# Optimization experiments

Hardware: AMD Instinct MI355X
Metric: run time of the kernel (lower is better)

The kernel has to match this reference:

```python
import jax, jax.numpy as jnp
import numpy as np

N_NODES = 100000
N_EDGES = 1600000
N_GRAPHS = 1000
D_IN = 64
D_HID = 64
D_OUT = 8


def _glorot(k, shape):
    lim = float(np.sqrt(6.0 / (shape[0] + shape[1])))
    return jax.random.uniform(k, shape, jnp.float32, -lim, lim)


def setup_inputs() -> dict:
    key = jax.random.key(0)
    ks = jax.random.split(key, 12)
    x = jax.random.normal(ks[0], (N_NODES, D_IN), jnp.float32)
    edge_index = jax.random.randint(ks[1], (2, N_EDGES), 0, N_NODES, jnp.int32)
    batch = jnp.sort(jax.random.randint(ks[2], (N_NODES,), 0, N_GRAPHS, jnp.int32))
    return {
        "x": x,
        "edge_index": edge_index,
        "batch": batch,
        "W1": _glorot(ks[3], (D_IN, D_HID)),
        "b1": jnp.zeros((D_HID,), jnp.float32),
        "W2": _glorot(ks[4], (D_HID, D_HID)),
        "b2": jnp.zeros((D_HID,), jnp.float32),
        "lw1": _glorot(ks[5], (D_HID, D_HID // 2)),
        "lb1": jnp.zeros((D_HID // 2,), jnp.float32),
        "lw2": _glorot(ks[6], (D_HID // 2, D_OUT)),
        "lb2": jnp.zeros((D_OUT,), jnp.float32),
    }


def reference(x, edge_index, batch, W1, b1, W2, b2, lw1, lb1, lw2, lb2):
    # --- GCN normalization (PyG defaults: add self-loops, sym norm) ---
    loop = jnp.arange(N_NODES, dtype=edge_index.dtype)
    src = jnp.concatenate([edge_index[0], loop])
    dst = jnp.concatenate([edge_index[1], loop])
    deg = jax.ops.segment_sum(jnp.ones_like(dst, jnp.float32), dst, num_segments=N_NODES)
    dinv = jnp.where(deg > 0, jax.lax.rsqrt(jnp.maximum(deg, 1.0)), 0.0)
    norm = dinv[src] * dinv[dst]  # [E+N]

    def gcn_conv(h, W, b):
        h = h @ W  # [N, d]
        msg = h[src] * norm[:, None]  # gather along edges
        return jax.ops.segment_sum(msg, dst, num_segments=N_NODES) + b

    h = jax.nn.relu(gcn_conv(x, W1, b1))
    h = gcn_conv(h, W2, b2)

    # --- global mean pool per graph ---
    counts = jax.ops.segment_sum(jnp.ones((N_NODES,), jnp.float32), batch, num_segments=N_GRAPHS)
    pooled = jax.ops.segment_sum(h, batch, num_segments=N_GRAPHS) / jnp.maximum(counts, 1.0)[:, None]

    # --- MLP head (dropout = identity in eval) ---
    z = jax.nn.relu(pooled @ lw1 + lb1)
    return z @ lw2 + lb2
```

## Files before the change

### kernel.cpp

```cpp
#include <hip/hip_runtime.h>

static constexpr int NN  = 100000;
static constexpr int NE  = 1600000;
static constexpr int NG  = 1000;
static constexpr int D   = 64;
static constexpr int DH  = 32;
static constexpr int DO  = 8;
static constexpr int BKT = 128;
static constexpr int NBK = (NN + BKT - 1) / BKT;
static constexpr int CAP = 2560;
static constexpr int CHUNK = 4096;
static constexpr int NCH = (NE + CHUNK - 1) / CHUNK;

typedef __attribute__((ext_vector_type(8))) short bf16x8;
typedef __attribute__((ext_vector_type(4))) float f32x4;

__device__ __forceinline__ float b2f(unsigned short u) {
    return __uint_as_float(((unsigned int)u) << 16);
}
__device__ __forceinline__ unsigned short f2b(float f) {
    unsigned int u = __float_as_uint(f);
    u += 0x7FFFu + ((u >> 16) & 1u);
    return (unsigned short)(u >> 16);
}
__device__ __forceinline__ uint4 pack8(const unsigned short* h) {
    uint4 u;
    u.x = (unsigned)h[0] | ((unsigned)h[1] << 16);
    u.y = (unsigned)h[2] | ((unsigned)h[3] << 16);
    u.z = (unsigned)h[4] | ((unsigned)h[5] << 16);
    u.w = (unsigned)h[6] | ((unsigned)h[7] << 16);
    return u;
}

__global__ __launch_bounds__(256) void
k_prepw(const float* __restrict__ W1, const float* __restrict__ W2,
        unsigned short* __restrict__ wtbuf, int* __restrict__ gcur) {
    int t = threadIdx.x;
    if (blockIdx.x == 0) {
        for (int b = t; b < NBK; b += 256) gcur[b] = 0;
    } else {
        const float* W = (blockIdx.x == 2) ? W2 : W1;
        unsigned short* WtHi = wtbuf + (size_t)(blockIdx.x - 1) * 8192;
        unsigned short* WtLo = WtHi + 4096;
        int n = t >> 2, k0 = (t & 3) * 16;
        unsigned short hi[16], lo[16];
#pragma unroll
        for (int i = 0; i < 16; ++i) {
            float v = W[(k0 + i) * 64 + n];
            hi[i] = f2b(v);
            lo[i] = f2b(v - b2f(hi[i]));
        }
        ((uint4*)WtHi)[n * 8 + (t & 3) * 2]     = pack8(hi);
        ((uint4*)WtHi)[n * 8 + (t & 3) * 2 + 1] = pack8(hi + 8);
        ((uint4*)WtLo)[n * 8 + (t & 3) * 2]     = pack8(lo);
        ((uint4*)WtLo)[n * 8 + (t & 3) * 2 + 1] = pack8(lo + 8);
    }
}

__global__ __launch_bounds__(512) void
k_bin(const int* __restrict__ src, const int* __restrict__ dst,
      int* __restrict__ gcur, int* __restrict__ ebuf) {
    __shared__ int lcnt[NBK];
    __shared__ int lbase[NBK];
    int t = threadIdx.x;
    long base = (long)blockIdx.x * CHUNK;
    for (int b = t; b < NBK; b += 512) lcnt[b] = 0;
    __syncthreads();
    int pk[8], bk[8], of[8];
#pragma unroll
    for (int j = 0; j < 8; ++j) {
        long i = base + j * 512 + t;
        if (i < NE) {
            int d = dst[i];
            bk[j] = d >> 7;
            pk[j] = src[i] * BKT + (d & (BKT - 1));
            of[j] = atomicAdd(&lcnt[bk[j]], 1);
        } else bk[j] = -1;
    }
    __syncthreads();
    for (int b = t; b < NBK; b += 512) {
        int c = lcnt[b];
        if (c) lbase[b] = b * CAP + atomicAdd(&gcur[b], c);
    }
    __syncthreads();
#pragma unroll
    for (int j = 0; j < 8; ++j)
        if (bk[j] >= 0) ebuf[lbase[bk[j]] + of[j]] = pk[j];
}

__global__ __launch_bounds__(512) void
k_csrdeg(const int* __restrict__ gcur, const int* __restrict__ ebuf,
         int* __restrict__ rowptr, int* __restrict__ deg, float* __restrict__ dinv,
         int* __restrict__ csr) {
    __shared__ int hist[BKT];
    __shared__ int sc[BKT];
    __shared__ int lcur[BKT];
    int b = blockIdx.x, t = threadIdx.x;
    if (t < BKT) hist[t] = 0;
    __syncthreads();
    int beg = b * CAP;
    int end = beg + gcur[b];
    for (int e = beg + t; e < end; e += 512)
        atomicAdd(&hist[ebuf[e] & (BKT - 1)], 1);
    __syncthreads();
    if (t < BKT) sc[t] = hist[t];
    __syncthreads();
    for (int o = 1; o < BKT; o <<= 1) {
        int a = (t < BKT && t >= o) ? sc[t - o] : 0;
        __syncthreads();
        if (t < BKT) sc[t] += a;
        __syncthreads();
    }
    int v0 = b * BKT;
    if (t < BKT) {
        int v = v0 + t;
        if (v < NN) {
            int excl = beg + sc[t] - hist[t];
            rowptr[v] = excl;
            deg[v]    = hist[t];
            dinv[v]   = rsqrtf((float)(hist[t] + 1));
            lcur[t]   = excl;
        }
    }
    __syncthreads();
    for (int e = beg + t; e < end; e += 512) {
        int p = ebuf[e];
        int slot = atomicAdd(&lcur[p & (BKT - 1)], 1);
        csr[slot] = p >> 7;
    }
}

__global__ __launch_bounds__(256) void
k_mm_mfma(const float* __restrict__ Ain, const unsigned short* __restrict__ wt,
          const float* __restrict__ dinv, uint4* __restrict__ out) {
    __shared__ unsigned short smem[4 * 64 * 72];
    unsigned short* Ahi  = smem;
    unsigned short* Alo  = smem + 4608;
    unsigned short* WtHi = smem + 9216;
    unsigned short* WtLo = smem + 13824;
    int t = threadIdx.x;
    int r = t >> 2, cc = t & 3, c0 = cc * 16;
    long n0 = (long)blockIdx.x * 64;
    {
        const uint4* H = (const uint4*)wt;
        const uint4* L = (const uint4*)(wt + 4096);
        uint4* dh = (uint4*)&WtHi[r * 72 + c0];
        uint4* dl = (uint4*)&WtLo[r * 72 + c0];
        dh[0] = H[r * 8 + cc * 2]; dh[1] = H[r * 8 + cc * 2 + 1];
        dl[0] = L[r * 8 + cc * 2]; dl[1] = L[r * 8 + cc * 2 + 1];
    }
    {
        long n = n0 + r; if (n >= NN) n = NN - 1;
        const float4* X = (const float4*)Ain;
        unsigned short hi[16], lo[16];
#pragma unroll
        for (int i = 0; i < 4; ++i) {
            float4 v = X[n * 16 + cc * 4 + i];
            float vv[4] = {v.x, v.y, v.z, v.w};
#pragma unroll
            for (int j = 0; j < 4; ++j) {
                unsigned short h = f2b(vv[j]);
                hi[i * 4 + j] = h;
                lo[i * 4 + j] = f2b(vv[j] - b2f(h));
            }
        }
        uint4* dh = (uint4*)&Ahi[r * 72 + c0];
        uint4* dl = (uint4*)&Alo[r * 72 + c0];
        dh[0] = pack8(hi); dh[1] = pack8(hi + 8);
        dl[0] = pack8(lo); dl[1] = pack8(lo + 8);
    }
    __syncthreads();
    int lane = t & 63, w = t >> 6;
    int q = lane >> 4, m = lane & 15;
    f32x4 acc[4] = {{0.f,0.f,0.f,0.f},{0.f,0.f,0.f,0.f},{0.f,0.f,0.f,0.f},{0.f,0.f,0.f,0.f}};
#pragma unroll
    for (int s = 0; s < 2; ++s) {
        int ko = s * 32 + q * 8;
        bf16x8 ah = *(const bf16x8*)&Ahi[(w * 16 + m) * 72 + ko];
        bf16x8 al = *(const bf16x8*)&Alo[(w * 16 + m) * 72 + ko];
#pragma unroll
        for (int c = 0; c < 4; ++c) {
            bf16x8 bh = *(const bf16x8*)&WtHi[(c * 16 + m) * 72 + ko];
            bf16x8 bl = *(const bf16x8*)&WtLo[(c * 16 + m) * 72 + ko];
            acc[c] = __builtin_amdgcn_mfma_f32_16x16x32_bf16(ah, bh, acc[c], 0, 0, 0);
            acc[c] = __builtin_amdgcn_mfma_f32_16x16x32_bf16(ah, bl, acc[c], 0, 0, 0);
            acc[c] = __builtin_amdgcn_mfma_f32_16x16x32_bf16(al, bh, acc[c], 0, 0, 0);
        }
    }
    __syncthreads();
    float* Ct = (float*)smem;
#pragma unroll
    for (int c = 0; c < 4; ++c)
#pragma unroll
        for (int rr = 0; rr < 4; ++rr)
            Ct[(w * 16 + q * 4 + rr) * 68 + c * 16 + m] = acc[c][rr];
    __syncthreads();
    {
        long n = n0 + r;
        if (n < NN) {
            float dv = dinv[n];
            unsigned short ob[16];
#pragma unroll
            for (int i = 0; i < 4; ++i) {
                float4 v = *(const float4*)&Ct[r * 68 + c0 + i * 4];
                ob[i * 4 + 0] = f2b(v.x * dv); ob[i * 4 + 1] = f2b(v.y * dv);
                ob[i * 4 + 2] = f2b(v.z * dv); ob[i * 4 + 3] = f2b(v.w * dv);
            }
            out[n * 8 + cc * 2]     = pack8(ob);
            out[n * 8 + cc * 2 + 1] = pack8(ob + 8);
        }
    }
}

__global__ __launch_bounds__(512) void
k_aggmm(const int* __restrict__ rowptr, const int* __restrict__ deg,
        const int* __restrict__ csr,
        const uint4* __restrict__ g4, const float* __restrict__ dinv,
        const float* __restrict__ bias, const unsigned short* __restrict__ wt,
        uint4* __restrict__ out) {
    __shared__ unsigned short smem[3 * 4608];
    unsigned short* Ahi  = smem;
    unsigned short* WtHi = smem + 4608;
    unsigned short* WtLo = smem + 9216;
    int t = threadIdx.x;
    long n0 = (long)blockIdx.x * 64;
    if (t < 256) {
        int r = t >> 2, cc = t & 3, c0 = cc * 16;
        const uint4* H = (const uint4*)wt;
        const uint4* L = (const uint4*)(wt + 4096);
        uint4* dh = (uint4*)&WtHi[r * 72 + c0];
        uint4* dl = (uint4*)&WtLo[r * 72 + c0];
        dh[0] = H[r * 8 + cc * 2]; dh[1] = H[r * 8 + cc * 2 + 1];
        dl[0] = L[r * 8 + cc * 2]; dl[1] = L[r * 8 + cc * 2 + 1];
    }
    int lane = t & 63, w = t >> 6;
    int fg = lane & 7, slot = lane >> 3;
    int ln = w * 8 + slot;
    long v = n0 + ln;
    int vc = (v < NN) ? (int)v : NN - 1;
    int beg = rowptr[vc];
    int len = (v < NN) ? deg[vc] : 0;
    int lmax = len;
    lmax = max(lmax, __shfl_xor(lmax, 8));
    lmax = max(lmax, __shfl_xor(lmax, 16));
    lmax = max(lmax, __shfl_xor(lmax, 32));
    float acc[8];
    {
        uint4 sv = g4[(long)vc * 8 + fg];
        if (v >= NN) { sv.x = sv.y = sv.z = sv.w = 0u; }
        acc[0] = __uint_as_float(sv.x << 16); acc[1] = __uint_as_float(sv.x & 0xFFFF0000u);
        acc[2] = __uint_as_float(sv.y << 16); acc[3] = __uint_as_float(sv.y & 0xFFFF0000u);
        acc[4] = __uint_as_float(sv.z << 16); acc[5] = __uint_as_float(sv.z & 0xFFFF0000u);
        acc[6] = __uint_as_float(sv.w << 16); acc[7] = __uint_as_float(sv.w & 0xFFFF0000u);
    }
    for (int e = 0; e < lmax; e += 8) {
#pragma unroll
        for (int j = 0; j < 8; ++j) {
            int ee = e + j;
            float m = (ee < len) ? 1.f : 0.f;
            int idx = beg + ((ee < len) ? ee : 0);
            int srcn = csr[idx];
            uint4 a = g4[(long)srcn * 8 + fg];
            acc[0] += m * __uint_as_float(a.x << 16);
            acc[1] += m * __uint_as_float(a.x & 0xFFFF0000u);
            acc[2] += m * __uint_as_float(a.y << 16);
            acc[3] += m * __uint_as_float(a.y & 0xFFFF0000u);
            acc[4] += m * __uint_as_float(a.z << 16);
            acc[5] += m * __uint_as_float(a.z & 0xFFFF0000u);
            acc[6] += m * __uint_as_float(a.w << 16);
            acc[7] += m * __uint_as_float(a.w & 0xFFFF0000u);
        }
    }
    {
        float dv = dinv[vc];
        unsigned short ob[8];
#pragma unroll
        for (int k = 0; k < 8; ++k) {
            float x = fmaxf(acc[k] * dv + bias[fg * 8 + k], 0.f);
            ob[k] = f2b(x);
        }
        *(uint4*)&Ahi[ln * 72 + fg * 8] = pack8(ob);
    }
    __syncthreads();
    int q = lane >> 4, m = lane & 15;
    int rs = (w & 3) * 16;
    int cb0 = (w >> 2) * 2;
    f32x4 c2[2] = {{0.f,0.f,0.f,0.f},{0.f,0.f,0.f,0.f}};
#pragma unroll
    for (int s = 0; s < 2; ++s) {
        int ko = s * 32 + q * 8;
        bf16x8 ah = *(const bf16x8*)&Ahi[(rs + m) * 72 + ko];
#pragma unroll
        for (int c = 0; c < 2; ++c) {
            bf16x8 bh = *(const bf16x8*)&WtHi[((cb0 + c) * 16 + m) * 72 + ko];
            bf16x8 bl = *(const bf16x8*)&WtLo[((cb0 + c) * 16 + m) * 72 + ko];
            c2[c] = __builtin_amdgcn_mfma_f32_16x16x32_bf16(ah, bh, c2[c], 0, 0, 0);
            c2[c] = __builtin_amdgcn_mfma_f32_16x16x32_bf16(ah, bl, c2[c], 0, 0, 0);
        }
    }
    __syncthreads();
    float* Ct = (float*)smem;
#pragma unroll
    for (int c = 0; c < 2; ++c)
#pragma unroll
        for (int rr = 0; rr < 4; ++rr)
            Ct[(rs + q * 4 + rr) * 68 + (cb0 + c) * 16 + m] = c2[c][rr];
    __syncthreads();
    {
        int r = t >> 3, c8 = (t & 7) * 8;
        long n = n0 + r;
        if (n < NN) {
            float dv = dinv[n];
            float4 a = *(const float4*)&Ct[r * 68 + c8];
            float4 b = *(const float4*)&Ct[r * 68 + c8 + 4];
            unsigned short ob[8] = {f2b(a.x * dv), f2b(a.y * dv), f2b(a.z * dv), f2b(a.w * dv),
                                    f2b(b.x * dv), f2b(b.y * dv), f2b(b.z * dv), f2b(b.w * dv)};
            out[n * 8 + (t & 7)] = pack8(ob);
        }
    }
}

__global__ __launch_bounds__(256) void
k_agg2(const int* __restrict__ rowptr, const int* __restrict__ deg,
       const int* __restrict__ csr,
       const uint4* __restrict__ g4, const float* __restrict__ dinv,
       const float* __restrict__ bias, uint4* __restrict__ out4) {
    int t = threadIdx.x;
    int lane = t & 63;
    int fg = lane & 7;
    int slot = lane >> 3;
    int wid = blockIdx.x * 4 + (t >> 6);
    int v = wid * 8 + slot;
    int beg = rowptr[v];
    int len = deg[v];
    int lmax = len;
    lmax = max(lmax, __shfl_xor(lmax, 8));
    lmax = max(lmax, __shfl_xor(lmax, 16));
    lmax = max(lmax, __shfl_xor(lmax, 32));
    float acc[8];
    {
        uint4 sv = g4[(long)v * 8 + fg];
        acc[0] = __uint_as_float(sv.x << 16); acc[1] = __uint_as_float(sv.x & 0xFFFF0000u);
        acc[2] = __uint_as_float(sv.y << 16); acc[3] = __uint_as_float(sv.y & 0xFFFF0000u);
        acc[4] = __uint_as_float(sv.z << 16); acc[5] = __uint_as_float(sv.z & 0xFFFF0000u);
        acc[6] = __uint_as_float(sv.w << 16); acc[7] = __uint_as_float(sv.w & 0xFFFF0000u);
    }
    for (int e = 0; e < lmax; e += 8) {
#pragma unroll
        for (int j = 0; j < 8; ++j) {
            int ee = e + j;
            float m = (ee < len) ? 1.f : 0.f;
            int idx = beg + ((ee < len) ? ee : 0);
            int srcn = csr[idx];
            uint4 a = g4[(long)srcn * 8 + fg];
            acc[0] += m * __uint_as_float(a.x << 16);
            acc[1] += m * __uint_as_float(a.x & 0xFFFF0000u);
            acc[2] += m * __uint_as_float(a.y << 16);
            acc[3] += m * __uint_as_float(a.y & 0xFFFF0000u);
            acc[4] += m * __uint_as_float(a.z << 16);
            acc[5] += m * __uint_as_float(a.z & 0xFFFF0000u);
            acc[6] += m * __uint_as_float(a.w << 16);
            acc[7] += m * __uint_as_float(a.w & 0xFFFF0000u);
        }
    }
    float dv = dinv[v];
    unsigned short ob[8];
#pragma unroll
    for (int k = 0; k < 8; ++k)
        ob[k] = f2b(acc[k] * dv + bias[fg * 8 + k]);
    out4[(long)v * 8 + fg] = pack8(ob);
}

__global__ void k_poolhead(const unsigned short* __restrict__ h,
                           const int* __restrict__ batch,
                           const float* __restrict__ lw1, const float* __restrict__ lb1,
                           const float* __restrict__ lw2, const float* __restrict__ lb2,
                           float* __restrict__ out) {
    __shared__ float pl[D];
    __shared__ float z[DH];
    int g = blockIdx.x;
    int t = threadIdx.x;
    int lo = 0, hi = NN;
    while (lo < hi) { int m = (lo + hi) >> 1; if (batch[m] < g) lo = m + 1; else hi = m; }
    int lb = lo;
    hi = NN;
    while (lo < hi) { int m = (lo + hi) >> 1; if (batch[m] < g + 1) lo = m + 1; else hi = m; }
    int ub = lo;
    float s = 0.f;
    int n = lb;
    for (; n + 4 <= ub; n += 4) {
        float a0 = b2f(h[(long)(n + 0) * D + t]);
        float a1 = b2f(h[(long)(n + 1) * D + t]);
        float a2 = b2f(h[(long)(n + 2) * D + t]);
        float a3 = b2f(h[(long)(n + 3) * D + t]);
        s += a0 + a1 + a2 + a3;
    }
    for (; n < ub; ++n) s += b2f(h[(long)n * D + t]);
    pl[t] = s / fmaxf((float)(ub - lb), 1.0f);
    __syncthreads();
    if (t < DH) {
        float a = lb1[t];
#pragma unroll
        for (int k = 0; k < D; ++k) a += pl[k] * lw1[k * DH + t];
        z[t] = fmaxf(a, 0.f);
    }
    __syncthreads();
    if (t < DO) {
        float a = lb2[t];
#pragma unroll
        for (int j = 0; j < DH; ++j) a += z[j] * lw2[j * DO + t];
        out[g * DO + t] = a;
    }
}

extern "C" void kernel_launch(void* const* d_in, const int* in_sizes, int n_in,
                              void* d_out, int out_size, void* d_ws, size_t ws_size,
                              hipStream_t stream) {
    const float* x    = (const float*)d_in[0];
    const int*   ei   = (const int*)  d_in[1];
    const int*   batch= (const int*)  d_in[2];
    const float* W1   = (const float*)d_in[3];
    const float* b1   = (const float*)d_in[4];
    const float* W2   = (const float*)d_in[5];
    const float* b2   = (const float*)d_in[6];
    const float* lw1  = (const float*)d_in[7];
    const float* lb1  = (const float*)d_in[8];
    const float* lw2  = (const float*)d_in[9];
    const float* lb2  = (const float*)d_in[10];
    float* out = (float*)d_out;

    const int* srcv = ei;
    const int* dstv = ei + NE;

    char* ws = (char*)d_ws;
    size_t off = 0;
    auto alloc = [&](size_t bytes) {
        void* p = ws + off;
        off = (off + bytes + 255) & ~(size_t)255;
        return p;
    };
    int*   gcur   = (int*)  alloc((size_t)NBK * 4);
    int*   rowptr = (int*)  alloc((size_t)NN * 4);
    int*   deg    = (int*)  alloc((size_t)NN * 4);
    int*   csr    = (int*)  alloc((size_t)NBK * CAP * 4);
    float* dinv   = (float*)alloc((size_t)NN * 4);
    unsigned short* wtbuf = (unsigned short*)alloc((size_t)4 * 4096 * 2);
    unsigned short* bufA = (unsigned short*)alloc((size_t)NN * D * 2);
    unsigned short* bufB = (unsigned short*)alloc((size_t)NN * D * 2);
    int*   ebuf   = (int*)bufA;

    k_prepw <<<3, 256, 0, stream>>>(W1, W2, wtbuf, gcur);
    k_bin   <<<NCH, 512, 0, stream>>>(srcv, dstv, gcur, ebuf);
    k_csrdeg<<<NBK, 512, 0, stream>>>(gcur, ebuf, rowptr, deg, dinv, csr);

    const int MMB = (NN + 63) / 64;

    k_mm_mfma<<<MMB, 256, 0, stream>>>(x, wtbuf, dinv, (uint4*)bufA);
    k_aggmm<<<MMB, 512, 0, stream>>>(rowptr, deg, csr, (const uint4*)bufA, dinv, b1,
                                     wtbuf + 8192, (uint4*)bufB);
    k_agg2<<<NN / 32, 256, 0, stream>>>(rowptr, deg, csr, (const uint4*)bufB, dinv, b2,
                                        (uint4*)bufA);
    k_poolhead<<<NG, 64, 0, stream>>>(bufA, batch, lw1, lb1, lw2, lb2, out);
}
```

Measured before the change: 213.6 us.

## Sort nodes by degree within graphs and fuse second aggregation with mean pooling

Adds a per-graph counting sort of nodes by in-degree so that each wavefront in the aggregation kernels processes nodes of similar degree, reducing divergence from the padded lmax loop. The second aggregation now scales by dinv and accumulates directly into a pooled fp32 buffer with wave-level reduction and atomics, which removes the bf16 h2 write and the separate pool pass; b2 is folded into the head. This costs an extra sort kernel, indirect perm lookups, scattered output writes, and float atomics whose summation order is nondeterministic.

```diff
diff --git a/kernel.cpp b/kernel.cpp
--- a/kernel.cpp
+++ b/kernel.cpp
@@ -34,10 +34,16 @@
 
 __global__ __launch_bounds__(256) void
 k_prepw(const float* __restrict__ W1, const float* __restrict__ W2,
-        unsigned short* __restrict__ wtbuf, int* __restrict__ gcur) {
+        unsigned short* __restrict__ wtbuf, int* __restrict__ gcur,
+        float* __restrict__ pooled) {
     int t = threadIdx.x;
     if (blockIdx.x == 0) {
         for (int b = t; b < NBK; b += 256) gcur[b] = 0;
+    } else if (blockIdx.x >= 3) {
+        int b = blockIdx.x - 3;
+        float4 z4 = {0.f, 0.f, 0.f, 0.f};
+        for (int i = b * 256 + t; i < NG * D / 4; i += 8 * 256)
+            ((float4*)pooled)[i] = z4;
     } else {
         const float* W = (blockIdx.x == 2) ? W2 : W1;
         unsigned short* WtHi = wtbuf + (size_t)(blockIdx.x - 1) * 8192;
@@ -127,6 +133,45 @@
         int p = ebuf[e];
         int slot = atomicAdd(&lcur[p & (BKT - 1)], 1);
         csr[slot] = p >> 7;
+    }
+}
+
+__global__ __launch_bounds__(256) void
+k_gsort(const int* __restrict__ batch, const int* __restrict__ deg,
+        int* __restrict__ perm, int* __restrict__ cnts) {
+    __shared__ int hist[64];
+    __shared__ int scan[64];
+    __shared__ int bnd[2];
+    int g = blockIdx.x, t = threadIdx.x;
+    if (t < 2) {
+        int tgt = g + t;
+        int lo = 0, hi = NN;
+        while (lo < hi) { int m = (lo + hi) >> 1; if (batch[m] < tgt) lo = m + 1; else hi = m; }
+        bnd[t] = lo;
+    }
+    if (t < 64) hist[t] = 0;
+    __syncthreads();
+    int lb = bnd[0], ub = bnd[1], cnt = ub - lb;
+    if (t == 0) cnts[g] = cnt;
+    for (int i = t; i < cnt; i += 256) {
+        int d = deg[lb + i]; if (d > 63) d = 63;
+        atomicAdd(&hist[d], 1);
+    }
+    __syncthreads();
+    if (t < 64) scan[t] = hist[t];
+    __syncthreads();
+    for (int o = 1; o < 64; o <<= 1) {
+        int a = (t < 64 && t >= o) ? scan[t - o] : 0;
+        __syncthreads();
+        if (t < 64) scan[t] += a;
+        __syncthreads();
+    }
+    if (t < 64) hist[t] = scan[t] - hist[t];
+    __syncthreads();
+    for (int i = t; i < cnt; i += 256) {
+        int d = deg[lb + i]; if (d > 63) d = 63;
+        int pos = atomicAdd(&hist[d], 1);
+        perm[lb + pos] = lb + i;
     }
 }
 
@@ -217,7 +262,7 @@
         const int* __restrict__ csr,
         const uint4* __restrict__ g4, const float* __restrict__ dinv,
         const float* __restrict__ bias, const unsigned short* __restrict__ wt,
-        uint4* __restrict__ out) {
+        const int* __restrict__ perm, uint4* __restrict__ out) {
     __shared__ unsigned short smem[3 * 4608];
     unsigned short* Ahi  = smem;
     unsigned short* WtHi = smem + 4608;
@@ -237,7 +282,7 @@
     int fg = lane & 7, slot = lane >> 3;
     int ln = w * 8 + slot;
     long v = n0 + ln;
-    int vc = (v < NN) ? (int)v : NN - 1;
+    int vc = (v < NN) ? perm[v] : 0;
     int beg = rowptr[vc];
     int len = (v < NN) ? deg[vc] : 0;
     int lmax = len;
@@ -310,27 +355,29 @@
         int r = t >> 3, c8 = (t & 7) * 8;
         long n = n0 + r;
         if (n < NN) {
-            float dv = dinv[n];
+            int node = perm[n];
+            float dv = dinv[node];
             float4 a = *(const float4*)&Ct[r * 68 + c8];
             float4 b = *(const float4*)&Ct[r * 68 + c8 + 4];
             unsigned short ob[8] = {f2b(a.x * dv), f2b(a.y * dv), f2b(a.z * dv), f2b(a.w * dv),
                                     f2b(b.x * dv), f2b(b.y * dv), f2b(b.z * dv), f2b(b.w * dv)};
-            out[n * 8 + (t & 7)] = pack8(ob);
+            out[(long)node * 8 + (t & 7)] = pack8(ob);
         }
     }
 }
 
 __global__ __launch_bounds__(256) void
-k_agg2(const int* __restrict__ rowptr, const int* __restrict__ deg,
-       const int* __restrict__ csr,
-       const uint4* __restrict__ g4, const float* __restrict__ dinv,
-       const float* __restrict__ bias, uint4* __restrict__ out4) {
+k_agg2pool(const int* __restrict__ rowptr, const int* __restrict__ deg,
+           const int* __restrict__ csr,
+           const uint4* __restrict__ g4, const float* __restrict__ dinv,
+           const int* __restrict__ perm, const int* __restrict__ batch,
+           float* __restrict__ pooled) {
     int t = threadIdx.x;
     int lane = t & 63;
     int fg = lane & 7;
     int slot = lane >> 3;
-    int wid = blockIdx.x * 4 + (t >> 6);
-    int v = wid * 8 + slot;
+    int idx = blockIdx.x * 32 + (t >> 6) * 8 + slot;
+    int v = perm[idx];
     int beg = rowptr[v];
     int len = deg[v];
     int lmax = len;
@@ -350,8 +397,8 @@
         for (int j = 0; j < 8; ++j) {
             int ee = e + j;
             float m = (ee < len) ? 1.f : 0.f;
-            int idx = beg + ((ee < len) ? ee : 0);
-            int srcn = csr[idx];
+            int idx2 = beg + ((ee < len) ? ee : 0);
+            int srcn = csr[idx2];
             uint4 a = g4[(long)srcn * 8 + fg];
             acc[0] += m * __uint_as_float(a.x << 16);
             acc[1] += m * __uint_as_float(a.x & 0xFFFF0000u);
@@ -364,39 +411,40 @@
         }
     }
     float dv = dinv[v];
-    unsigned short ob[8];
-#pragma unroll
-    for (int k = 0; k < 8; ++k)
-        ob[k] = f2b(acc[k] * dv + bias[fg * 8 + k]);
-    out4[(long)v * 8 + fg] = pack8(ob);
-}
-
-__global__ void k_poolhead(const unsigned short* __restrict__ h,
-                           const int* __restrict__ batch,
-                           const float* __restrict__ lw1, const float* __restrict__ lb1,
-                           const float* __restrict__ lw2, const float* __restrict__ lb2,
-                           float* __restrict__ out) {
+#pragma unroll
+    for (int k = 0; k < 8; ++k) acc[k] *= dv;
+    int g = batch[v];
+    int g0 = __shfl(g, 0), g7 = __shfl(g, 63);
+    if (g0 == g7) {
+#pragma unroll
+        for (int k = 0; k < 8; ++k) {
+            acc[k] += __shfl_xor(acc[k], 8);
+            acc[k] += __shfl_xor(acc[k], 16);
+            acc[k] += __shfl_xor(acc[k], 32);
+        }
+        if (slot == 0) {
+#pragma unroll
+            for (int k = 0; k < 8; ++k)
+                atomicAdd(&pooled[g0 * D + fg * 8 + k], acc[k]);
+        }
+    } else {
+#pragma unroll
+        for (int k = 0; k < 8; ++k)
+            atomicAdd(&pooled[g * D + fg * 8 + k], acc[k]);
+    }
+}
+
+__global__ void k_head(const float* __restrict__ pooled, const int* __restrict__ cnts,
+                       const float* __restrict__ b2,
+                       const float* __restrict__ lw1, const float* __restrict__ lb1,
+                       const float* __restrict__ lw2, const float* __restrict__ lb2,
+                       float* __restrict__ out) {
     __shared__ float pl[D];
     __shared__ float z[DH];
     int g = blockIdx.x;
     int t = threadIdx.x;
-    int lo = 0, hi = NN;
-    while (lo < hi) { int m = (lo + hi) >> 1; if (batch[m] < g) lo = m + 1; else hi = m; }
-    int lb = lo;
-    hi = NN;
-    while (lo < hi) { int m = (lo + hi) >> 1; if (batch[m] < g + 1) lo = m + 1; else hi = m; }
-    int ub = lo;
-    float s = 0.f;
-    int n = lb;
-    for (; n + 4 <= ub; n += 4) {
-        float a0 = b2f(h[(long)(n + 0) * D + t]);
-        float a1 = b2f(h[(long)(n + 1) * D + t]);
-        float a2 = b2f(h[(long)(n + 2) * D + t]);
-        float a3 = b2f(h[(long)(n + 3) * D + t]);
-        s += a0 + a1 + a2 + a3;
-    }
-    for (; n < ub; ++n) s += b2f(h[(long)n * D + t]);
-    pl[t] = s / fmaxf((float)(ub - lb), 1.0f);
+    int c = cnts[g];
+    pl[t] = (c > 0) ? (pooled[g * D + t] / (float)c + b2[t]) : 0.f;
     __syncthreads();
     if (t < DH) {
         float a = lb1[t];
@@ -444,21 +492,25 @@
     int*   deg    = (int*)  alloc((size_t)NN * 4);
     int*   csr    = (int*)  alloc((size_t)NBK * CAP * 4);
     float* dinv   = (float*)alloc((size_t)NN * 4);
+    int*   perm   = (int*)  alloc((size_t)NN * 4);
+    int*   cnts   = (int*)  alloc((size_t)NG * 4);
+    float* pooled = (float*)alloc((size_t)NG * D * 4);
     unsigned short* wtbuf = (unsigned short*)alloc((size_t)4 * 4096 * 2);
     unsigned short* bufA = (unsigned short*)alloc((size_t)NN * D * 2);
     unsigned short* bufB = (unsigned short*)alloc((size_t)NN * D * 2);
     int*   ebuf   = (int*)bufA;
 
-    k_prepw <<<3, 256, 0, stream>>>(W1, W2, wtbuf, gcur);
+    k_prepw <<<11, 256, 0, stream>>>(W1, W2, wtbuf, gcur, pooled);
     k_bin   <<<NCH, 512, 0, stream>>>(srcv, dstv, gcur, ebuf);
     k_csrdeg<<<NBK, 512, 0, stream>>>(gcur, ebuf, rowptr, deg, dinv, csr);
+    k_gsort <<<NG, 256, 0, stream>>>(batch, deg, perm, cnts);
 
     const int MMB = (NN + 63) / 64;
 
     k_mm_mfma<<<MMB, 256, 0, stream>>>(x, wtbuf, dinv, (uint4*)bufA);
     k_aggmm<<<MMB, 512, 0, stream>>>(rowptr, deg, csr, (const uint4*)bufA, dinv, b1,
-                                     wtbuf + 8192, (uint4*)bufB);
-    k_agg2<<<NN / 32, 256, 0, stream>>>(rowptr, deg, csr, (const uint4*)bufB, dinv, b2,
-                                        (uint4*)bufA);
-    k_poolhead<<<NG, 64, 0, stream>>>(bufA, batch, lw1, lb1, lw2, lb2, out);
-}
+                                     wtbuf + 8192, perm, (uint4*)bufB);
+    k_agg2pool<<<NN / 32, 256, 0, stream>>>(rowptr, deg, csr, (const uint4*)bufB, dinv,
+                                            perm, batch, pooled);
+    k_head<<<NG, 64, 0, stream>>>(pooled, cnts, b2, lw1, lb1, lw2, lb2, out);
+}
```

After: 244.8 us. 1.15x slower.

## Fuse second GCN aggregation with per-graph mean pooling via graph-aligned wave map

Applied to the files above, without the earlier changes.

Builds a map assigning nodes to waves so each 8-node wave group belongs to a single graph (padded with -1), computed from batch boundaries in the prep kernel plus a new fill kernel. The second aggregation then reduces its 8 node results per wave with shuffles and writes a per-wave partial sum, and the head kernel sums partials per graph and adds the bias. This removes the bf16 write and reread of the full second-layer output and the per-graph binary searches in the pooling kernel. In exchange it adds an extra launch, padding waves, and a fixed MAXW capacity that assumes the padded wave count fits.

```diff
diff --git a/kernel.cpp b/kernel.cpp
--- a/kernel.cpp
+++ b/kernel.cpp
@@ -11,6 +11,8 @@
 static constexpr int CAP = 2560;
 static constexpr int CHUNK = 4096;
 static constexpr int NCH = (NE + CHUNK - 1) / CHUNK;
+static constexpr int MAXW = 13504;
+static constexpr int MAPS = MAXW * 8;
 
 typedef __attribute__((ext_vector_type(8))) short bf16x8;
 typedef __attribute__((ext_vector_type(4))) float f32x4;
@@ -32,29 +34,85 @@
     return u;
 }
 
-__global__ __launch_bounds__(256) void
+__global__ __launch_bounds__(1024) void
 k_prepw(const float* __restrict__ W1, const float* __restrict__ W2,
-        unsigned short* __restrict__ wtbuf, int* __restrict__ gcur) {
+        const int* __restrict__ batch,
+        unsigned short* __restrict__ wtbuf, int* __restrict__ gcur,
+        int* __restrict__ lbg, int* __restrict__ wbase, int* __restrict__ map) {
+    __shared__ int bnd[NG + 1];
+    __shared__ int tsum[256];
     int t = threadIdx.x;
-    if (blockIdx.x == 0) {
-        for (int b = t; b < NBK; b += 256) gcur[b] = 0;
+    int b = blockIdx.x;
+    if (b == 0) {
+        for (int i = t; i < NBK; i += 1024) gcur[i] = 0;
+    } else if (b == 3) {
+        for (int g = t; g <= NG; g += 1024) {
+            int lo = 0, hi = NN;
+            while (lo < hi) { int m = (lo + hi) >> 1; if (batch[m] < g) lo = m + 1; else hi = m; }
+            bnd[g] = lo;
+        }
+        __syncthreads();
+        int s = 0, loc[4];
+        if (t < 256) {
+#pragma unroll
+            for (int j = 0; j < 4; ++j) {
+                int g = t * 4 + j;
+                int pw = (g < NG) ? ((bnd[g + 1] - bnd[g] + 7) >> 3) : 0;
+                loc[j] = s; s += pw;
+            }
+            tsum[t] = s;
+        }
+        __syncthreads();
+        for (int o = 1; o < 256; o <<= 1) {
+            int a = (t < 256 && t >= o) ? tsum[t - o] : 0;
+            __syncthreads();
+            if (t < 256) tsum[t] += a;
+            __syncthreads();
+        }
+        if (t < 256) {
+            int base = (t > 0) ? tsum[t - 1] : 0;
+#pragma unroll
+            for (int j = 0; j < 4; ++j) {
+                int g = t * 4 + j;
+                if (g < NG) wbase[g] = base + loc[j];
+            }
+            if (t == 255) wbase[NG] = tsum[255];
+        }
+        if (t <= NG) lbg[t] = bnd[t];
+    } else if (b >= 4) {
+        int4 m4 = {-1, -1, -1, -1};
+        for (int i = (b - 4) * 1024 + t; i < MAPS / 4; i += 8 * 1024)
+            ((int4*)map)[i] = m4;
     } else {
-        const float* W = (blockIdx.x == 2) ? W2 : W1;
-        unsigned short* WtHi = wtbuf + (size_t)(blockIdx.x - 1) * 8192;
-        unsigned short* WtLo = WtHi + 4096;
-        int n = t >> 2, k0 = (t & 3) * 16;
-        unsigned short hi[16], lo[16];
-#pragma unroll
-        for (int i = 0; i < 16; ++i) {
-            float v = W[(k0 + i) * 64 + n];
-            hi[i] = f2b(v);
-            lo[i] = f2b(v - b2f(hi[i]));
-        }
-        ((uint4*)WtHi)[n * 8 + (t & 3) * 2]     = pack8(hi);
-        ((uint4*)WtHi)[n * 8 + (t & 3) * 2 + 1] = pack8(hi + 8);
-        ((uint4*)WtLo)[n * 8 + (t & 3) * 2]     = pack8(lo);
-        ((uint4*)WtLo)[n * 8 + (t & 3) * 2 + 1] = pack8(lo + 8);
-    }
+        if (t < 256) {
+            const float* W = (b == 2) ? W2 : W1;
+            unsigned short* WtHi = wtbuf + (size_t)(b - 1) * 8192;
+            unsigned short* WtLo = WtHi + 4096;
+            int n = t >> 2, k0 = (t & 3) * 16;
+            unsigned short hi[16], lo[16];
+#pragma unroll
+            for (int i = 0; i < 16; ++i) {
+                float v = W[(k0 + i) * 64 + n];
+                hi[i] = f2b(v);
+                lo[i] = f2b(v - b2f(hi[i]));
+            }
+            ((uint4*)WtHi)[n * 8 + (t & 3) * 2]     = pack8(hi);
+            ((uint4*)WtHi)[n * 8 + (t & 3) * 2 + 1] = pack8(hi + 8);
+            ((uint4*)WtLo)[n * 8 + (t & 3) * 2]     = pack8(lo);
+            ((uint4*)WtLo)[n * 8 + (t & 3) * 2 + 1] = pack8(lo + 8);
+        }
+    }
+}
+
+__global__ __launch_bounds__(128) void
+k_fillmap(const int* __restrict__ lbg, const int* __restrict__ wbase,
+          int* __restrict__ map) {
+    int g = blockIdx.x;
+    int base = wbase[g] * 8;
+    int lb = lbg[g], n = lbg[g + 1] - lb;
+    int padded = (n + 7) & ~7;
+    for (int i = threadIdx.x; i < padded; i += 128)
+        map[base + i] = (i < n) ? (lb + i) : -1;
 }
 
 __global__ __launch_bounds__(512) void
@@ -321,25 +379,27 @@
 }
 
 __global__ __launch_bounds__(256) void
-k_agg2(const int* __restrict__ rowptr, const int* __restrict__ deg,
-       const int* __restrict__ csr,
-       const uint4* __restrict__ g4, const float* __restrict__ dinv,
-       const float* __restrict__ bias, uint4* __restrict__ out4) {
+k_agg2pool(const int* __restrict__ rowptr, const int* __restrict__ deg,
+           const int* __restrict__ csr,
+           const uint4* __restrict__ g4, const float* __restrict__ dinv,
+           const int* __restrict__ map, float* __restrict__ partial) {
     int t = threadIdx.x;
     int lane = t & 63;
     int fg = lane & 7;
     int slot = lane >> 3;
-    int wid = blockIdx.x * 4 + (t >> 6);
-    int v = wid * 8 + slot;
-    int beg = rowptr[v];
-    int len = deg[v];
+    int w = blockIdx.x * 4 + (t >> 6);
+    int v = map[w * 8 + slot];
+    int vc = (v < 0) ? 0 : v;
+    int beg = rowptr[vc];
+    int len = (v < 0) ? 0 : deg[vc];
     int lmax = len;
     lmax = max(lmax, __shfl_xor(lmax, 8));
     lmax = max(lmax, __shfl_xor(lmax, 16));
     lmax = max(lmax, __shfl_xor(lmax, 32));
     float acc[8];
     {
-        uint4 sv = g4[(long)v * 8 + fg];
+        uint4 sv = g4[(long)vc * 8 + fg];
+        if (v < 0) { sv.x = sv.y = sv.z = sv.w = 0u; }
         acc[0] = __uint_as_float(sv.x << 16); acc[1] = __uint_as_float(sv.x & 0xFFFF0000u);
         acc[2] = __uint_as_float(sv.y << 16); acc[3] = __uint_as_float(sv.y & 0xFFFF0000u);
         acc[4] = __uint_as_float(sv.z << 16); acc[5] = __uint_as_float(sv.z & 0xFFFF0000u);
@@ -350,8 +410,8 @@
         for (int j = 0; j < 8; ++j) {
             int ee = e + j;
             float m = (ee < len) ? 1.f : 0.f;
-            int idx = beg + ((ee < len) ? ee : 0);
-            int srcn = csr[idx];
+            int idx2 = beg + ((ee < len) ? ee : 0);
+            int srcn = csr[idx2];
             uint4 a = g4[(long)srcn * 8 + fg];
             acc[0] += m * __uint_as_float(a.x << 16);
             acc[1] += m * __uint_as_float(a.x & 0xFFFF0000u);
@@ -363,40 +423,38 @@
             acc[7] += m * __uint_as_float(a.w & 0xFFFF0000u);
         }
     }
-    float dv = dinv[v];
-    unsigned short ob[8];
-#pragma unroll
-    for (int k = 0; k < 8; ++k)
-        ob[k] = f2b(acc[k] * dv + bias[fg * 8 + k]);
-    out4[(long)v * 8 + fg] = pack8(ob);
-}
-
-__global__ void k_poolhead(const unsigned short* __restrict__ h,
-                           const int* __restrict__ batch,
-                           const float* __restrict__ lw1, const float* __restrict__ lb1,
-                           const float* __restrict__ lw2, const float* __restrict__ lb2,
-                           float* __restrict__ out) {
+    float dv = dinv[vc];
+#pragma unroll
+    for (int k = 0; k < 8; ++k) {
+        acc[k] *= dv;
+        acc[k] += __shfl_xor(acc[k], 8);
+        acc[k] += __shfl_xor(acc[k], 16);
+        acc[k] += __shfl_xor(acc[k], 32);
+    }
+    if (slot == 0) {
+        float4* p4 = (float4*)&partial[(long)w * 64];
+        f32x4 a = {acc[0], acc[1], acc[2], acc[3]};
+        f32x4 b = {acc[4], acc[5], acc[6], acc[7]};
+        p4[fg * 2]     = *(float4*)&a;
+        p4[fg * 2 + 1] = *(float4*)&b;
+    }
+}
+
+__global__ void k_head(const float* __restrict__ partial,
+                       const int* __restrict__ lbg, const int* __restrict__ wbase,
+                       const float* __restrict__ b2,
+                       const float* __restrict__ lw1, const float* __restrict__ lb1,
+                       const float* __restrict__ lw2, const float* __restrict__ lb2,
+                       float* __restrict__ out) {
     __shared__ float pl[D];
     __shared__ float z[DH];
     int g = blockIdx.x;
     int t = threadIdx.x;
-    int lo = 0, hi = NN;
-    while (lo < hi) { int m = (lo + hi) >> 1; if (batch[m] < g) lo = m + 1; else hi = m; }
-    int lb = lo;
-    hi = NN;
-    while (lo < hi) { int m = (lo + hi) >> 1; if (batch[m] < g + 1) lo = m + 1; else hi = m; }
-    int ub = lo;
+    int w0 = wbase[g], w1 = wbase[g + 1];
+    int cnt = lbg[g + 1] - lbg[g];
     float s = 0.f;
-    int n = lb;
-    for (; n + 4 <= ub; n += 4) {
-        float a0 = b2f(h[(long)(n + 0) * D + t]);
-        float a1 = b2f(h[(long)(n + 1) * D + t]);
-        float a2 = b2f(h[(long)(n + 2) * D + t]);
-        float a3 = b2f(h[(long)(n + 3) * D + t]);
-        s += a0 + a1 + a2 + a3;
-    }
-    for (; n < ub; ++n) s += b2f(h[(long)n * D + t]);
-    pl[t] = s / fmaxf((float)(ub - lb), 1.0f);
+    for (int w = w0; w < w1; ++w) s += partial[(long)w * 64 + t];
+    pl[t] = (cnt > 0) ? (s / (float)cnt + b2[t]) : 0.f;
     __syncthreads();
     if (t < DH) {
         float a = lb1[t];
@@ -444,21 +502,26 @@
     int*   deg    = (int*)  alloc((size_t)NN * 4);
     int*   csr    = (int*)  alloc((size_t)NBK * CAP * 4);
     float* dinv   = (float*)alloc((size_t)NN * 4);
+    int*   lbg    = (int*)  alloc((size_t)(NG + 1) * 4);
+    int*   wbase  = (int*)  alloc((size_t)(NG + 1) * 4);
+    int*   map    = (int*)  alloc((size_t)MAPS * 4);
+    float* partial= (float*)alloc((size_t)MAXW * D * 4);
     unsigned short* wtbuf = (unsigned short*)alloc((size_t)4 * 4096 * 2);
     unsigned short* bufA = (unsigned short*)alloc((size_t)NN * D * 2);
     unsigned short* bufB = (unsigned short*)alloc((size_t)NN * D * 2);
     int*   ebuf   = (int*)bufA;
 
-    k_prepw <<<3, 256, 0, stream>>>(W1, W2, wtbuf, gcur);
-    k_bin   <<<NCH, 512, 0, stream>>>(srcv, dstv, gcur, ebuf);
-    k_csrdeg<<<NBK, 512, 0, stream>>>(gcur, ebuf, rowptr, deg, dinv, csr);
+    k_prepw  <<<12, 1024, 0, stream>>>(W1, W2, batch, wtbuf, gcur, lbg, wbase, map);
+    k_fillmap<<<NG, 128, 0, stream>>>(lbg, wbase, map);
+    k_bin    <<<NCH, 512, 0, stream>>>(srcv, dstv, gcur, ebuf);
+    k_csrdeg <<<NBK, 512, 0, stream>>>(gcur, ebuf, rowptr, deg, dinv, csr);
 
     const int MMB = (NN + 63) / 64;
 
     k_mm_mfma<<<MMB, 256, 0, stream>>>(x, wtbuf, dinv, (uint4*)bufA);
     k_aggmm<<<MMB, 512, 0, stream>>>(rowptr, deg, csr, (const uint4*)bufA, dinv, b1,
                                      wtbuf + 8192, (uint4*)bufB);
-    k_agg2<<<NN / 32, 256, 0, stream>>>(rowptr, deg, csr, (const uint4*)bufB, dinv, b2,
-                                        (uint4*)bufA);
-    k_poolhead<<<NG, 64, 0, stream>>>(bufA, batch, lw1, lb1, lw2, lb2, out);
-}
+    k_agg2pool<<<MAXW / 4, 256, 0, stream>>>(rowptr, deg, csr, (const uint4*)bufB, dinv,
+                                             map, partial);
+    k_head<<<NG, 64, 0, stream>>>(partial, lbg, wbase, b2, lw1, lb1, lw2, lb2, out);
+}
```

After: 212.9 us. Within noise of the previous version (-0.3%).
